# Kernel tuning notes

Hardware: AMD Instinct MI355X
Metric: run time of the kernel (lower is better)

## Reference

```python
import jax, jax.numpy as jnp
import numpy as np

N_NODES = 100000


def gcn_conv(x, src, dst, W, b, n_nodes):
    """PyG GCNConv: add self-loops, symmetric deg^{-1/2} norm, gather-scatter."""
    h = x @ W  # [N, out]
    # add self-loops (fixed shapes)
    loop = jnp.arange(n_nodes, dtype=src.dtype)
    s = jnp.concatenate([src, loop])
    d = jnp.concatenate([dst, loop])
    # degree on destination (includes self-loop)
    deg = jax.ops.segment_sum(jnp.ones_like(d, dtype=h.dtype), d, num_segments=n_nodes)
    dinv = jnp.where(deg > 0, jax.lax.rsqrt(deg), 0.0)
    norm = dinv[s] * dinv[d]  # [E+N]
    msg = h[s] * norm[:, None]  # gather + scale, [E+N, out]
    out = jax.ops.segment_sum(msg, d, num_segments=n_nodes)  # scatter-add
    return out + b


def setup_inputs() -> dict:
    key = jax.random.key(0)
    ks = jax.random.split(key, 10)
    n, in_d, hid, out_d, e = N_NODES, 64, 128, 64, 1600000
    x = jax.random.normal(ks[0], (n, in_d), dtype=jnp.float32)
    edge_index = jax.random.randint(ks[1], (2, e), 0, n, dtype=jnp.int64)
    s = 0.05
    return {
        "x": x,
        "edge_index": edge_index,
        "W1": jax.random.normal(ks[2], (in_d, hid), dtype=jnp.float32) * s,
        "b1": jnp.zeros((hid,), dtype=jnp.float32),
        "W2": jax.random.normal(ks[3], (hid, out_d), dtype=jnp.float32) * s,
        "b2": jnp.zeros((out_d,), dtype=jnp.float32),
        "Wd": jax.random.normal(ks[4], (out_d, 1), dtype=jnp.float32) * s,
        "bd": jnp.zeros((1,), dtype=jnp.float32),
        "Wp": jax.random.normal(ks[5], (out_d, 1), dtype=jnp.float32) * s,
        "bp": jnp.zeros((1,), dtype=jnp.float32),
    }


def reference(x, edge_index, W1, b1, W2, b2, Wd, bd, Wp, bp):
    src, dst = edge_index[0], edge_index[1]
    n = x.shape[0]
    h = jax.nn.relu(gcn_conv(x, src, dst, W1, b1, n))
    h = jax.nn.relu(gcn_conv(h, src, dst, W2, b2, n))
    duration_out = h @ Wd + bd  # [N, 1]
    phase_out = h @ Wp + bp     # [N, 1]
    return (duration_out, phase_out)
```

## Files before the change

kernel.cpp:

```cpp
#include <hip/hip_runtime.h>
#include <cstdint>
#include <cstddef>


#define MAXC 512
#define CAP  6144
#define SEG  3456
#define GPAD 16

typedef __attribute__((ext_vector_type(8))) short bf16x8;
typedef __attribute__((ext_vector_type(4))) float f32x4;

__device__ __forceinline__ float blo(unsigned int u) {
  return __uint_as_float(u << 16);
}
__device__ __forceinline__ float bhi(unsigned int u) {
  return __uint_as_float(u & 0xffff0000u);
}
__device__ __forceinline__ unsigned short f2b(float f) {
  unsigned int u = __float_as_uint(f);
  unsigned int r = u + 0x7fffu + ((u >> 16) & 1u);
  return (unsigned short)(r >> 16);
}

__device__ __forceinline__ void gacc(const uint2* __restrict__ tab,
                                     const int* __restrict__ cp,
                                     int m, int q, float4& acc) {
  int nfull = m & ~7;
  int t = 0;
  if (nfull) {
    int cb[8];
#pragma unroll
    for (int i = 0; i < 8; ++i) cb[i] = cp[i];
    for (t = 0; t < nfull; t += 8) {
      int ca[8];
#pragma unroll
      for (int i = 0; i < 8; ++i) ca[i] = cb[i];
      int tn = t + 8;
      if (tn < nfull) {
#pragma unroll
        for (int i = 0; i < 8; ++i) cb[i] = cp[tn + i];
      }
      uint2 v[8];
#pragma unroll
      for (int i = 0; i < 8; ++i) v[i] = tab[(size_t)ca[i] * 16 + q];
      acc.x += ((blo(v[0].x) + blo(v[1].x)) + (blo(v[2].x) + blo(v[3].x)))
             + ((blo(v[4].x) + blo(v[5].x)) + (blo(v[6].x) + blo(v[7].x)));
      acc.y += ((bhi(v[0].x) + bhi(v[1].x)) + (bhi(v[2].x) + bhi(v[3].x)))
             + ((bhi(v[4].x) + bhi(v[5].x)) + (bhi(v[6].x) + bhi(v[7].x)));
      acc.z += ((blo(v[0].y) + blo(v[1].y)) + (blo(v[2].y) + blo(v[3].y)))
             + ((blo(v[4].y) + blo(v[5].y)) + (blo(v[6].y) + blo(v[7].y)));
      acc.w += ((bhi(v[0].y) + bhi(v[1].y)) + (bhi(v[2].y) + bhi(v[3].y)))
             + ((bhi(v[4].y) + bhi(v[5].y)) + (bhi(v[6].y) + bhi(v[7].y)));
    }
  }
  if (t + 4 <= m) {
    int i0 = cp[t], i1 = cp[t + 1], i2 = cp[t + 2], i3 = cp[t + 3];
    uint2 v0 = tab[(size_t)i0 * 16 + q], v1 = tab[(size_t)i1 * 16 + q];
    uint2 v2 = tab[(size_t)i2 * 16 + q], v3 = tab[(size_t)i3 * 16 + q];
    acc.x += (blo(v0.x) + blo(v1.x)) + (blo(v2.x) + blo(v3.x));
    acc.y += (bhi(v0.x) + bhi(v1.x)) + (bhi(v2.x) + bhi(v3.x));
    acc.z += (blo(v0.y) + blo(v1.y)) + (blo(v2.y) + blo(v3.y));
    acc.w += (bhi(v0.y) + bhi(v1.y)) + (bhi(v2.y) + bhi(v3.y));
    t += 4;
  }
  for (; t < m; ++t) {
    int i0 = cp[t];
    uint2 v0 = tab[(size_t)i0 * 16 + q];
    acc.x += blo(v0.x); acc.y += bhi(v0.x);
    acc.z += blo(v0.y); acc.w += bhi(v0.y);
  }
}

__global__ void k_binit(int* __restrict__ gcur, int nc) {
  int b = blockIdx.x * 256 + threadIdx.x;
  if (b < nc) gcur[b * GPAD] = b * CAP;
}

__global__ __launch_bounds__(256) void k_pass1(const int* __restrict__ src,
                                               const int* __restrict__ dst,
                                               int* __restrict__ gcur,
                                               int* __restrict__ P,
                                               int E, int nc, int seg) {
  __shared__ int hist[MAXC];
  __shared__ int lofs[MAXC];
  __shared__ int base[MAXC];
  __shared__ int sbuf[SEG];
  __shared__ unsigned short dbuf[SEG];
  __shared__ int ssc[256];
  int tid = threadIdx.x;
  int start = blockIdx.x * seg;
  int end = min(E, start + seg);
  int cnt = end - start;
  if (cnt <= 0) return;
  for (int i = tid; i < MAXC; i += 256) hist[i] = 0;
  __syncthreads();
  for (int i = start + tid; i < end; i += 256)
    atomicAdd(&hist[dst[i] >> 8], 1);
  __syncthreads();
  int p0 = hist[2 * tid], p1 = hist[2 * tid + 1];
  int ps = p0 + p1;
  ssc[tid] = ps;
  __syncthreads();
  for (int off = 1; off < 256; off <<= 1) {
    int t = (tid >= off) ? ssc[tid - off] : 0;
    __syncthreads();
    ssc[tid] += t;
    __syncthreads();
  }
  int pe = ssc[tid] - ps;
  lofs[2 * tid] = pe;
  lofs[2 * tid + 1] = pe + p0;
  __syncthreads();
  for (int b = tid; b < nc; b += 256) {
    int h = hist[b];
    base[b] = (h ? atomicAdd(&gcur[b * GPAD], h) : 0) - lofs[b];
  }
  __syncthreads();
  for (int i = tid; i < MAXC; i += 256) hist[i] = lofs[i];
  __syncthreads();
  for (int i = start + tid; i < end; i += 256) {
    int d = dst[i];
    int b = d >> 8;
    int r = atomicAdd(&hist[b], 1);
    sbuf[r] = src[i] | ((d & 255) << 17);
    dbuf[r] = (unsigned short)b;
  }
  __syncthreads();
  for (int j = tid; j < cnt; j += 256) {
    P[base[dbuf[j]] + j] = sbuf[j];
  }
}

__global__ __launch_bounds__(256) void k_pass2(const int* __restrict__ P,
                                               const int* __restrict__ gcur,
                                               int* __restrict__ rs,
                                               int* __restrict__ c,
                                               float* __restrict__ dinv,
                                               int* __restrict__ col,
                                               const float* __restrict__ x,
                                               unsigned int* __restrict__ xh,
                                               int N) {
  __shared__ int sh[256];
  __shared__ int lcur[256];
  __shared__ float sdi[256];
  int tid = threadIdx.x;
  int node0 = blockIdx.x << 8;
  int begin = blockIdx.x * CAP;
  int end = gcur[blockIdx.x * GPAD];
  sh[tid] = 0;
  __syncthreads();
  for (int i = begin + tid; i < end; i += 256)
    atomicAdd(&sh[P[i] >> 17], 1);
  __syncthreads();
  int s = sh[tid];
  for (int off = 1; off < 256; off <<= 1) {
    int t = (tid >= off) ? sh[tid - off] : 0;
    __syncthreads();
    sh[tid] += t;
    __syncthreads();
  }
  int excl = sh[tid] - s;
  int node = node0 + tid;
  float di = rsqrtf((float)(s + 1));
  sdi[tid] = di;
  if (node < N) {
    rs[node] = begin + excl;
    c[node] = s;
    dinv[node] = di;
  }
  lcur[tid] = begin + excl;
  __syncthreads();
  for (int i = begin + tid; i < end; i += 256) {
    int p = P[i];
    int pos = atomicAdd(&lcur[p >> 17], 1);
    col[pos] = p & 0x1FFFF;
  }
  int nrem = min(256, N - node0);
  if (nrem <= 0) return;
  for (int i = tid; i < nrem * 16; i += 256) {
    int r = i >> 4, qq = i & 15;
    float d2 = sdi[r];
    float4 v = reinterpret_cast<const float4*>(x)[(size_t)(node0 + r) * 16 + qq];
    uint2 o;
    o.x = (unsigned int)f2b(v.x * d2) | ((unsigned int)f2b(v.y * d2) << 16);
    o.y = (unsigned int)f2b(v.z * d2) | ((unsigned int)f2b(v.w * d2) << 16);
    reinterpret_cast<uint2*>(xh)[(size_t)(node0 + r) * 16 + qq] = o;
  }
}

__global__ __launch_bounds__(256) void k_pull1(const unsigned int* __restrict__ xh,
                                               const int* __restrict__ rs,
                                               const int* __restrict__ cnt,
                                               const int* __restrict__ col,
                                               const float* __restrict__ dinv,
                                               unsigned int* __restrict__ aggh,
                                               int n) {
  int tid = threadIdx.x;
  int q = tid & 15;
  int node = (blockIdx.x * 256 + tid) >> 4;
  bool valid = node < n;
  int nidx = valid ? node : 0;
  int start = rs[nidx];
  int m = valid ? cnt[nidx] : 0;
  const uint2* xr = reinterpret_cast<const uint2*>(xh);
  float4 acc = {0.f, 0.f, 0.f, 0.f};
  gacc(xr, col + start, m, q, acc);
  if (valid) {
    uint2 sv = xr[(size_t)node * 16 + q];
    acc.x += blo(sv.x); acc.y += bhi(sv.x);
    acc.z += blo(sv.y); acc.w += bhi(sv.y);
    float di = dinv[node];
    uint2 o;
    o.x = (unsigned int)f2b(acc.x * di) | ((unsigned int)f2b(acc.y * di) << 16);
    o.y = (unsigned int)f2b(acc.z * di) | ((unsigned int)f2b(acc.w * di) << 16);
    reinterpret_cast<uint2*>(aggh)[(size_t)node * 16 + q] = o;
  }
}

#define OFF_W1T 16384
#define OFF_W2T 32768
#define OFF_H1  49152
__global__ __launch_bounds__(256) void k_gemm12(
    const unsigned int* __restrict__ aggh,
    const float* __restrict__ W1, const float* __restrict__ b1,
    const float* __restrict__ W2, const float* __restrict__ dinv,
    unsigned int* __restrict__ g2h, int n) {
  __shared__ __align__(16) char smem[81920];
  int tid = threadIdx.x;
  int lane = tid & 63;
  int wid = tid >> 6;
  int lr = lane & 15, lg = lane >> 4;
  int wr = wid >> 1, wc = wid & 1;
  {
    int nrow = tid >> 1, h = tid & 1;
    unsigned int pk[16];
#pragma unroll
    for (int q = 0; q < 16; ++q) {
      unsigned short a = f2b(W1[(size_t)(h * 32 + 2 * q) * 128 + nrow]);
      unsigned short bq = f2b(W1[(size_t)(h * 32 + 2 * q + 1) * 128 + nrow]);
      pk[q] = (unsigned int)a | ((unsigned int)bq << 16);
    }
#pragma unroll
    for (int cc = 0; cc < 4; ++cc) {
      uint4 v = make_uint4(pk[cc * 4], pk[cc * 4 + 1], pk[cc * 4 + 2], pk[cc * 4 + 3]);
      int byte = nrow * 128 + ((h * 64 + cc * 16) ^ ((nrow & 7) << 4));
      *reinterpret_cast<uint4*>(smem + OFF_W1T + byte) = v;
    }
  }
  {
    int nrow = tid >> 2, qt = tid & 3;
    unsigned int pk[16];
#pragma unroll
    for (int q = 0; q < 16; ++q) {
      unsigned short a = f2b(W2[(size_t)(qt * 32 + 2 * q) * 64 + nrow]);
      unsigned short bq = f2b(W2[(size_t)(qt * 32 + 2 * q + 1) * 64 + nrow]);
      pk[q] = (unsigned int)a | ((unsigned int)bq << 16);
    }
#pragma unroll
    for (int cc = 0; cc < 4; ++cc) {
      uint4 v = make_uint4(pk[cc * 4], pk[cc * 4 + 1], pk[cc * 4 + 2], pk[cc * 4 + 3]);
      int byte = nrow * 256 + ((qt * 64 + cc * 16) ^ ((nrow & 7) << 4));
      *reinterpret_cast<uint4*>(smem + OFF_W2T + byte) = v;
    }
  }
  float bias[4];
#pragma unroll
  for (int ni = 0; ni < 4; ++ni) bias[ni] = b1[wc * 64 + ni * 16 + lr];

  int ntiles = (n + 127) >> 7;
  for (int tile = blockIdx.x; tile < ntiles; tile += gridDim.x) {
    int row0 = tile << 7;
    __syncthreads();
#pragma unroll
    for (int j = 0; j < 4; ++j) {
      int idx = tid + 256 * j;
      int r = idx >> 3, u = idx & 7;
      uint4 v = make_uint4(0u, 0u, 0u, 0u);
      int row = row0 + r;
      if (row < n) v = reinterpret_cast<const uint4*>(aggh)[(size_t)row * 8 + u];
      int byte = r * 128 + ((u * 16) ^ ((r & 7) << 4));
      *reinterpret_cast<uint4*>(smem + byte) = v;
    }
    __syncthreads();
    f32x4 acc1[4][4];
#pragma unroll
    for (int mi = 0; mi < 4; ++mi)
#pragma unroll
      for (int ni = 0; ni < 4; ++ni) {
        f32x4 z = {0.f, 0.f, 0.f, 0.f};
        acc1[mi][ni] = z;
      }
#pragma unroll
    for (int kk = 0; kk < 2; ++kk) {
      int kb = kk * 64 + lg * 16;
      bf16x8 af[4], bfq[4];
#pragma unroll
      for (int mi = 0; mi < 4; ++mi) {
        int r = wr * 64 + mi * 16 + lr;
        af[mi] = *reinterpret_cast<const bf16x8*>(smem + r * 128 + (kb ^ ((r & 7) << 4)));
      }
#pragma unroll
      for (int ni = 0; ni < 4; ++ni) {
        int nr = wc * 64 + ni * 16 + lr;
        bfq[ni] = *reinterpret_cast<const bf16x8*>(smem + OFF_W1T + nr * 128 + (kb ^ ((nr & 7) << 4)));
      }
#pragma unroll
      for (int mi = 0; mi < 4; ++mi)
#pragma unroll
        for (int ni = 0; ni < 4; ++ni)
          acc1[mi][ni] = __builtin_amdgcn_mfma_f32_16x16x32_bf16(
              af[mi], bfq[ni], acc1[mi][ni], 0, 0, 0);
    }
#pragma unroll
    for (int mi = 0; mi < 4; ++mi) {
      int m0 = wr * 64 + mi * 16 + lg * 4;
#pragma unroll
      for (int ni = 0; ni < 4; ++ni) {
        int kcol = wc * 64 + ni * 16 + lr;
#pragma unroll
        for (int rj = 0; rj < 4; ++rj) {
          float v = fmaxf(acc1[mi][ni][rj] + bias[ni], 0.f);
          int mm = m0 + rj;
          int byte = mm * 256 + ((kcol * 2) ^ ((mm & 15) << 4));
          *reinterpret_cast<unsigned short*>(smem + OFF_H1 + byte) = f2b(v);
        }
      }
    }
    __syncthreads();
    f32x4 acc2[4][2];
#pragma unroll
    for (int mi = 0; mi < 4; ++mi)
#pragma unroll
      for (int ni = 0; ni < 2; ++ni) {
        f32x4 z = {0.f, 0.f, 0.f, 0.f};
        acc2[mi][ni] = z;
      }
#pragma unroll
    for (int kk = 0; kk < 4; ++kk) {
      int kb = kk * 64 + lg * 16;
      bf16x8 af[4], bfq[2];
#pragma unroll
      for (int mi = 0; mi < 4; ++mi) {
        int m = wr * 64 + mi * 16 + lr;
        af[mi] = *reinterpret_cast<const bf16x8*>(smem + OFF_H1 + m * 256 + (kb ^ ((m & 15) << 4)));
      }
#pragma unroll
      for (int ni = 0; ni < 2; ++ni) {
        int nr = wc * 32 + ni * 16 + lr;
        bfq[ni] = *reinterpret_cast<const bf16x8*>(smem + OFF_W2T + nr * 256 + (kb ^ ((nr & 7) << 4)));
      }
#pragma unroll
      for (int mi = 0; mi < 4; ++mi)
#pragma unroll
        for (int ni = 0; ni < 2; ++ni)
          acc2[mi][ni] = __builtin_amdgcn_mfma_f32_16x16x32_bf16(
              af[mi], bfq[ni], acc2[mi][ni], 0, 0, 0);
    }
    __syncthreads();
#pragma unroll
    for (int mi = 0; mi < 4; ++mi) {
      int m0 = wr * 64 + mi * 16 + lg * 4;
#pragma unroll
      for (int ni = 0; ni < 2; ++ni) {
        int nn = wc * 32 + ni * 16 + lr;
#pragma unroll
        for (int rj = 0; rj < 4; ++rj) {
          int mm = m0 + rj;
          int byte = mm * 256 + ((nn * 4) ^ ((mm & 15) << 4));
          *reinterpret_cast<float*>(smem + OFF_H1 + byte) = acc2[mi][ni][rj];
        }
      }
    }
    __syncthreads();
#pragma unroll
    for (int j = 0; j < 8; ++j) {
      int idx = tid + 256 * j;
      int r = idx >> 4, c4 = idx & 15;
      int row = row0 + r;
      if (row < n) {
        float4 v = *reinterpret_cast<const float4*>(
            smem + OFF_H1 + r * 256 + ((c4 * 16) ^ ((r & 15) << 4)));
        float di = dinv[row];
        uint2 o;
        o.x = (unsigned int)f2b(v.x * di) | ((unsigned int)f2b(v.y * di) << 16);
        o.y = (unsigned int)f2b(v.z * di) | ((unsigned int)f2b(v.w * di) << 16);
        reinterpret_cast<uint2*>(g2h)[(size_t)row * 16 + c4] = o;
      }
    }
  }
}

__global__ __launch_bounds__(256) void k_pull2(const unsigned int* __restrict__ g2h,
                                               const int* __restrict__ rs,
                                               const int* __restrict__ cnt,
                                               const int* __restrict__ col,
                                               const float* __restrict__ dinv,
                                               const float* __restrict__ b,
                                               const float* __restrict__ Wd,
                                               const float* __restrict__ Wp,
                                               const float* __restrict__ bd,
                                               const float* __restrict__ bp,
                                               float* __restrict__ out, int n) {
  int tid = threadIdx.x;
  int q = tid & 15;
  int node = (blockIdx.x * 256 + tid) >> 4;
  bool valid = node < n;
  int nidx = valid ? node : 0;
  int start = rs[nidx];
  int m = valid ? cnt[nidx] : 0;
  const uint2* gr = reinterpret_cast<const uint2*>(g2h);
  float4 acc = {0.f, 0.f, 0.f, 0.f};
  gacc(gr, col + start, m, q, acc);
  {
    uint2 sv = gr[(size_t)nidx * 16 + q];
    acc.x += blo(sv.x); acc.y += bhi(sv.x);
    acc.z += blo(sv.y); acc.w += bhi(sv.y);
  }
  float di = dinv[nidx];
  float4 b4 = *reinterpret_cast<const float4*>(b + q * 4);
  float4 wd4 = *reinterpret_cast<const float4*>(Wd + q * 4);
  float4 wp4 = *reinterpret_cast<const float4*>(Wp + q * 4);
  float vx = fmaxf(fmaf(acc.x, di, b4.x), 0.f);
  float vy = fmaxf(fmaf(acc.y, di, b4.y), 0.f);
  float vz = fmaxf(fmaf(acc.z, di, b4.z), 0.f);
  float vw = fmaxf(fmaf(acc.w, di, b4.w), 0.f);
  float dsum = vx * wd4.x + vy * wd4.y + vz * wd4.z + vw * wd4.w;
  float psum = vx * wp4.x + vy * wp4.y + vz * wp4.z + vw * wp4.w;
#pragma unroll
  for (int off = 1; off < 16; off <<= 1) {
    dsum += __shfl_xor(dsum, off);
    psum += __shfl_xor(psum, off);
  }
  if (valid && q == 0) {
    out[node] = dsum + bd[0];
    out[n + node] = psum + bp[0];
  }
}

extern "C" void kernel_launch(void* const* d_in, const int* in_sizes, int n_in,
                              void* d_out, int out_size, void* d_ws, size_t ws_size,
                              hipStream_t stream) {
  const float* x  = (const float*)d_in[0];
  const int*   ei = (const int*)d_in[1];
  const float* W1 = (const float*)d_in[2];
  const float* b1 = (const float*)d_in[3];
  const float* W2 = (const float*)d_in[4];
  const float* b2 = (const float*)d_in[5];
  const float* Wd = (const float*)d_in[6];
  const float* bd = (const float*)d_in[7];
  const float* Wp = (const float*)d_in[8];
  const float* bp = (const float*)d_in[9];
  float* out = (float*)d_out;

  const int N = in_sizes[0] / 64;
  const int E = in_sizes[1] / 2;
  const int* src = ei;
  const int* dst = ei + E;
  const int nc = (N + 255) >> 8;

  char* ws = (char*)d_ws;
  size_t off = 0;
  auto alloc = [&](size_t bytes) -> void* {
    size_t a = (off + 255) & ~(size_t)255;
    off = a + bytes;
    return (void*)(ws + a);
  };

  int*   gcur = (int*)alloc((size_t)MAXC * GPAD * 4);
  int*   rs   = (int*)alloc((size_t)N * 4);
  int*   c    = (int*)alloc((size_t)N * 4);
  float* dinv = (float*)alloc((size_t)N * 4);
  int*   P    = (int*)alloc((size_t)nc * CAP * 4);
  int*   col  = (int*)alloc((size_t)nc * CAP * 4);
  unsigned int* xh   = (unsigned int*)alloc((size_t)N * 64 * 2);
  unsigned int* aggh = (unsigned int*)alloc((size_t)N * 64 * 2);
  unsigned int* g2h  = (unsigned int*)alloc((size_t)N * 64 * 2);
  (void)ws_size; (void)n_in; (void)out_size;

  k_binit<<<(nc + 255) / 256, 256, 0, stream>>>(gcur, nc);

  int nb1 = 512;
  int seg = (E + nb1 - 1) / nb1;
  while (seg > SEG) { nb1 *= 2; seg = (E + nb1 - 1) / nb1; }
  k_pass1<<<nb1, 256, 0, stream>>>(src, dst, gcur, P, E, nc, seg);
  k_pass2<<<nc, 256, 0, stream>>>(P, gcur, rs, c, dinv, col, x, xh, N);

  k_pull1<<<(N + 15) / 16, 256, 0, stream>>>(xh, rs, c, col, dinv, aggh, N);
  k_gemm12<<<512, 256, 0, stream>>>(aggh, W1, b1, W2, dinv, g2h, N);
  k_pull2<<<(N + 15) / 16, 256, 0, stream>>>(g2h, rs, c, col, dinv, b2, Wd, Wp, bd, bp, out, N);
}
```

Before: 223.2 us.

## Widen gather loads to 16 bytes, use wave-shuffle scans, replace init kernel with memset

```diff
diff --git a/kernel.cpp b/kernel.cpp
--- a/kernel.cpp
+++ b/kernel.cpp
@@ -23,58 +23,52 @@
   return (unsigned short)(r >> 16);
 }
 
-__device__ __forceinline__ void gacc(const uint2* __restrict__ tab,
-                                     const int* __restrict__ cp,
-                                     int m, int q, float4& acc) {
-  int nfull = m & ~7;
+__device__ __forceinline__ void gacc8(const uint4* __restrict__ tab,
+                                      const int* __restrict__ cp,
+                                      int m, int q8, float a[8]) {
   int t = 0;
-  if (nfull) {
-    int cb[8];
-#pragma unroll
-    for (int i = 0; i < 8; ++i) cb[i] = cp[i];
-    for (t = 0; t < nfull; t += 8) {
-      int ca[8];
-#pragma unroll
-      for (int i = 0; i < 8; ++i) ca[i] = cb[i];
-      int tn = t + 8;
-      if (tn < nfull) {
-#pragma unroll
-        for (int i = 0; i < 8; ++i) cb[i] = cp[tn + i];
-      }
-      uint2 v[8];
-#pragma unroll
-      for (int i = 0; i < 8; ++i) v[i] = tab[(size_t)ca[i] * 16 + q];
-      acc.x += ((blo(v[0].x) + blo(v[1].x)) + (blo(v[2].x) + blo(v[3].x)))
-             + ((blo(v[4].x) + blo(v[5].x)) + (blo(v[6].x) + blo(v[7].x)));
-      acc.y += ((bhi(v[0].x) + bhi(v[1].x)) + (bhi(v[2].x) + bhi(v[3].x)))
-             + ((bhi(v[4].x) + bhi(v[5].x)) + (bhi(v[6].x) + bhi(v[7].x)));
-      acc.z += ((blo(v[0].y) + blo(v[1].y)) + (blo(v[2].y) + blo(v[3].y)))
-             + ((blo(v[4].y) + blo(v[5].y)) + (blo(v[6].y) + blo(v[7].y)));
-      acc.w += ((bhi(v[0].y) + bhi(v[1].y)) + (bhi(v[2].y) + bhi(v[3].y)))
-             + ((bhi(v[4].y) + bhi(v[5].y)) + (bhi(v[6].y) + bhi(v[7].y)));
-    }
-  }
-  if (t + 4 <= m) {
-    int i0 = cp[t], i1 = cp[t + 1], i2 = cp[t + 2], i3 = cp[t + 3];
-    uint2 v0 = tab[(size_t)i0 * 16 + q], v1 = tab[(size_t)i1 * 16 + q];
-    uint2 v2 = tab[(size_t)i2 * 16 + q], v3 = tab[(size_t)i3 * 16 + q];
-    acc.x += (blo(v0.x) + blo(v1.x)) + (blo(v2.x) + blo(v3.x));
-    acc.y += (bhi(v0.x) + bhi(v1.x)) + (bhi(v2.x) + bhi(v3.x));
-    acc.z += (blo(v0.y) + blo(v1.y)) + (blo(v2.y) + blo(v3.y));
-    acc.w += (bhi(v0.y) + bhi(v1.y)) + (bhi(v2.y) + bhi(v3.y));
-    t += 4;
+  for (; t + 8 <= m; t += 8) {
+    int c0 = cp[t],     c1 = cp[t + 1], c2 = cp[t + 2], c3 = cp[t + 3];
+    int c4 = cp[t + 4], c5 = cp[t + 5], c6 = cp[t + 6], c7 = cp[t + 7];
+    uint4 v0 = tab[(size_t)c0 * 8 + q8], v1 = tab[(size_t)c1 * 8 + q8];
+    uint4 v2 = tab[(size_t)c2 * 8 + q8], v3 = tab[(size_t)c3 * 8 + q8];
+    uint4 v4 = tab[(size_t)c4 * 8 + q8], v5 = tab[(size_t)c5 * 8 + q8];
+    uint4 v6 = tab[(size_t)c6 * 8 + q8], v7 = tab[(size_t)c7 * 8 + q8];
+    a[0] += ((blo(v0.x) + blo(v1.x)) + (blo(v2.x) + blo(v3.x)))
+          + ((blo(v4.x) + blo(v5.x)) + (blo(v6.x) + blo(v7.x)));
+    a[1] += ((bhi(v0.x) + bhi(v1.x)) + (bhi(v2.x) + bhi(v3.x)))
+          + ((bhi(v4.x) + bhi(v5.x)) + (bhi(v6.x) + bhi(v7.x)));
+    a[2] += ((blo(v0.y) + blo(v1.y)) + (blo(v2.y) + blo(v3.y)))
+          + ((blo(v4.y) + blo(v5.y)) + (blo(v6.y) + blo(v7.y)));
+    a[3] += ((bhi(v0.y) + bhi(v1.y)) + (bhi(v2.y) + bhi(v3.y)))
+          + ((bhi(v4.y) + bhi(v5.y)) + (bhi(v6.y) + bhi(v7.y)));
+    a[4] += ((blo(v0.z) + blo(v1.z)) + (blo(v2.z) + blo(v3.z)))
+          + ((blo(v4.z) + blo(v5.z)) + (blo(v6.z) + blo(v7.z)));
+    a[5] += ((bhi(v0.z) + bhi(v1.z)) + (bhi(v2.z) + bhi(v3.z)))
+          + ((bhi(v4.z) + bhi(v5.z)) + (bhi(v6.z) + bhi(v7.z)));
+    a[6] += ((blo(v0.w) + blo(v1.w)) + (blo(v2.w) + blo(v3.w)))
+          + ((blo(v4.w) + blo(v5.w)) + (blo(v6.w) + blo(v7.w)));
+    a[7] += ((bhi(v0.w) + bhi(v1.w)) + (bhi(v2.w) + bhi(v3.w)))
+          + ((bhi(v4.w) + bhi(v5.w)) + (bhi(v6.w) + bhi(v7.w)));
+  }
+  for (; t + 4 <= m; t += 4) {
+    int c0 = cp[t], c1 = cp[t + 1], c2 = cp[t + 2], c3 = cp[t + 3];
+    uint4 v0 = tab[(size_t)c0 * 8 + q8], v1 = tab[(size_t)c1 * 8 + q8];
+    uint4 v2 = tab[(size_t)c2 * 8 + q8], v3 = tab[(size_t)c3 * 8 + q8];
+    a[0] += (blo(v0.x) + blo(v1.x)) + (blo(v2.x) + blo(v3.x));
+    a[1] += (bhi(v0.x) + bhi(v1.x)) + (bhi(v2.x) + bhi(v3.x));
+    a[2] += (blo(v0.y) + blo(v1.y)) + (blo(v2.y) + blo(v3.y));
+    a[3] += (bhi(v0.y) + bhi(v1.y)) + (bhi(v2.y) + bhi(v3.y));
+    a[4] += (blo(v0.z) + blo(v1.z)) + (blo(v2.z) + blo(v3.z));
+    a[5] += (bhi(v0.z) + bhi(v1.z)) + (bhi(v2.z) + bhi(v3.z));
+    a[6] += (blo(v0.w) + blo(v1.w)) + (blo(v2.w) + blo(v3.w));
+    a[7] += (bhi(v0.w) + bhi(v1.w)) + (bhi(v2.w) + bhi(v3.w));
   }
   for (; t < m; ++t) {
-    int i0 = cp[t];
-    uint2 v0 = tab[(size_t)i0 * 16 + q];
-    acc.x += blo(v0.x); acc.y += bhi(v0.x);
-    acc.z += blo(v0.y); acc.w += bhi(v0.y);
-  }
-}
-
-__global__ void k_binit(int* __restrict__ gcur, int nc) {
-  int b = blockIdx.x * 256 + threadIdx.x;
-  if (b < nc) gcur[b * GPAD] = b * CAP;
+    uint4 v = tab[(size_t)cp[t] * 8 + q8];
+    a[0] += blo(v.x); a[1] += bhi(v.x); a[2] += blo(v.y); a[3] += bhi(v.y);
+    a[4] += blo(v.z); a[5] += bhi(v.z); a[6] += blo(v.w); a[7] += bhi(v.w);
+  }
 }
 
 __global__ __launch_bounds__(256) void k_pass1(const int* __restrict__ src,
@@ -87,8 +81,9 @@
   __shared__ int base[MAXC];
   __shared__ int sbuf[SEG];
   __shared__ unsigned short dbuf[SEG];
-  __shared__ int ssc[256];
+  __shared__ int wsum[4];
   int tid = threadIdx.x;
+  int lane = tid & 63, wv = tid >> 6;
   int start = blockIdx.x * seg;
   int end = min(E, start + seg);
   int cnt = end - start;
@@ -100,21 +95,26 @@
   __syncthreads();
   int p0 = hist[2 * tid], p1 = hist[2 * tid + 1];
   int ps = p0 + p1;
-  ssc[tid] = ps;
-  __syncthreads();
-  for (int off = 1; off < 256; off <<= 1) {
-    int t = (tid >= off) ? ssc[tid - off] : 0;
-    __syncthreads();
-    ssc[tid] += t;
-    __syncthreads();
-  }
-  int pe = ssc[tid] - ps;
+  int incl = ps;
+#pragma unroll
+  for (int off = 1; off < 64; off <<= 1) {
+    int t = __shfl_up(incl, off);
+    if (lane >= off) incl += t;
+  }
+  if (lane == 63) wsum[wv] = incl;
+  __syncthreads();
+  int addv = 0;
+#pragma unroll
+  for (int w = 0; w < 3; ++w)
+    if (w < wv) addv += wsum[w];
+  incl += addv;
+  int pe = incl - ps;
   lofs[2 * tid] = pe;
   lofs[2 * tid + 1] = pe + p0;
   __syncthreads();
   for (int b = tid; b < nc; b += 256) {
     int h = hist[b];
-    base[b] = (h ? atomicAdd(&gcur[b * GPAD], h) : 0) - lofs[b];
+    base[b] = (h ? (b * CAP + atomicAdd(&gcur[b * GPAD], h)) : 0) - lofs[b];
   }
   __syncthreads();
   for (int i = tid; i < MAXC; i += 256) hist[i] = lofs[i];
@@ -144,23 +144,32 @@
   __shared__ int sh[256];
   __shared__ int lcur[256];
   __shared__ float sdi[256];
+  __shared__ int wsum[4];
   int tid = threadIdx.x;
+  int lane = tid & 63, wv = tid >> 6;
   int node0 = blockIdx.x << 8;
   int begin = blockIdx.x * CAP;
-  int end = gcur[blockIdx.x * GPAD];
+  int end = begin + gcur[blockIdx.x * GPAD];
   sh[tid] = 0;
   __syncthreads();
   for (int i = begin + tid; i < end; i += 256)
     atomicAdd(&sh[P[i] >> 17], 1);
   __syncthreads();
   int s = sh[tid];
-  for (int off = 1; off < 256; off <<= 1) {
-    int t = (tid >= off) ? sh[tid - off] : 0;
-    __syncthreads();
-    sh[tid] += t;
-    __syncthreads();
-  }
-  int excl = sh[tid] - s;
+  int incl = s;
+#pragma unroll
+  for (int off = 1; off < 64; off <<= 1) {
+    int t = __shfl_up(incl, off);
+    if (lane >= off) incl += t;
+  }
+  if (lane == 63) wsum[wv] = incl;
+  __syncthreads();
+  int addv = 0;
+#pragma unroll
+  for (int w = 0; w < 3; ++w)
+    if (w < wv) addv += wsum[w];
+  incl += addv;
+  int excl = incl - s;
   int node = node0 + tid;
   float di = rsqrtf((float)(s + 1));
   sdi[tid] = di;
@@ -197,24 +206,26 @@
                                                unsigned int* __restrict__ aggh,
                                                int n) {
   int tid = threadIdx.x;
-  int q = tid & 15;
-  int node = (blockIdx.x * 256 + tid) >> 4;
+  int q8 = tid & 7;
+  int node = (blockIdx.x * 256 + tid) >> 3;
   bool valid = node < n;
   int nidx = valid ? node : 0;
   int start = rs[nidx];
   int m = valid ? cnt[nidx] : 0;
-  const uint2* xr = reinterpret_cast<const uint2*>(xh);
-  float4 acc = {0.f, 0.f, 0.f, 0.f};
-  gacc(xr, col + start, m, q, acc);
+  const uint4* xr = reinterpret_cast<const uint4*>(xh);
+  float a[8] = {0.f, 0.f, 0.f, 0.f, 0.f, 0.f, 0.f, 0.f};
+  gacc8(xr, col + start, m, q8, a);
   if (valid) {
-    uint2 sv = xr[(size_t)node * 16 + q];
-    acc.x += blo(sv.x); acc.y += bhi(sv.x);
-    acc.z += blo(sv.y); acc.w += bhi(sv.y);
+    uint4 sv = xr[(size_t)node * 8 + q8];
+    a[0] += blo(sv.x); a[1] += bhi(sv.x); a[2] += blo(sv.y); a[3] += bhi(sv.y);
+    a[4] += blo(sv.z); a[5] += bhi(sv.z); a[6] += blo(sv.w); a[7] += bhi(sv.w);
     float di = dinv[node];
-    uint2 o;
-    o.x = (unsigned int)f2b(acc.x * di) | ((unsigned int)f2b(acc.y * di) << 16);
-    o.y = (unsigned int)f2b(acc.z * di) | ((unsigned int)f2b(acc.w * di) << 16);
-    reinterpret_cast<uint2*>(aggh)[(size_t)node * 16 + q] = o;
+    uint4 o;
+    o.x = (unsigned int)f2b(a[0] * di) | ((unsigned int)f2b(a[1] * di) << 16);
+    o.y = (unsigned int)f2b(a[2] * di) | ((unsigned int)f2b(a[3] * di) << 16);
+    o.z = (unsigned int)f2b(a[4] * di) | ((unsigned int)f2b(a[5] * di) << 16);
+    o.w = (unsigned int)f2b(a[6] * di) | ((unsigned int)f2b(a[7] * di) << 16);
+    reinterpret_cast<uint4*>(aggh)[(size_t)node * 8 + q8] = o;
   }
 }
 
@@ -403,36 +414,45 @@
                                                const float* __restrict__ bp,
                                                float* __restrict__ out, int n) {
   int tid = threadIdx.x;
-  int q = tid & 15;
-  int node = (blockIdx.x * 256 + tid) >> 4;
+  int q8 = tid & 7;
+  int node = (blockIdx.x * 256 + tid) >> 3;
   bool valid = node < n;
   int nidx = valid ? node : 0;
   int start = rs[nidx];
   int m = valid ? cnt[nidx] : 0;
-  const uint2* gr = reinterpret_cast<const uint2*>(g2h);
-  float4 acc = {0.f, 0.f, 0.f, 0.f};
-  gacc(gr, col + start, m, q, acc);
+  const uint4* gr = reinterpret_cast<const uint4*>(g2h);
+  float a[8] = {0.f, 0.f, 0.f, 0.f, 0.f, 0.f, 0.f, 0.f};
+  gacc8(gr, col + start, m, q8, a);
   {
-    uint2 sv = gr[(size_t)nidx * 16 + q];
-    acc.x += blo(sv.x); acc.y += bhi(sv.x);
-    acc.z += blo(sv.y); acc.w += bhi(sv.y);
+    uint4 sv = gr[(size_t)nidx * 8 + q8];
+    a[0] += blo(sv.x); a[1] += bhi(sv.x); a[2] += blo(sv.y); a[3] += bhi(sv.y);
+    a[4] += blo(sv.z); a[5] += bhi(sv.z); a[6] += blo(sv.w); a[7] += bhi(sv.w);
   }
   float di = dinv[nidx];
-  float4 b4 = *reinterpret_cast<const float4*>(b + q * 4);
-  float4 wd4 = *reinterpret_cast<const float4*>(Wd + q * 4);
-  float4 wp4 = *reinterpret_cast<const float4*>(Wp + q * 4);
-  float vx = fmaxf(fmaf(acc.x, di, b4.x), 0.f);
-  float vy = fmaxf(fmaf(acc.y, di, b4.y), 0.f);
-  float vz = fmaxf(fmaf(acc.z, di, b4.z), 0.f);
-  float vw = fmaxf(fmaf(acc.w, di, b4.w), 0.f);
-  float dsum = vx * wd4.x + vy * wd4.y + vz * wd4.z + vw * wd4.w;
-  float psum = vx * wp4.x + vy * wp4.y + vz * wp4.z + vw * wp4.w;
-#pragma unroll
-  for (int off = 1; off < 16; off <<= 1) {
+  float4 bA = *reinterpret_cast<const float4*>(b + q8 * 8);
+  float4 bB = *reinterpret_cast<const float4*>(b + q8 * 8 + 4);
+  float4 wdA = *reinterpret_cast<const float4*>(Wd + q8 * 8);
+  float4 wdB = *reinterpret_cast<const float4*>(Wd + q8 * 8 + 4);
+  float4 wpA = *reinterpret_cast<const float4*>(Wp + q8 * 8);
+  float4 wpB = *reinterpret_cast<const float4*>(Wp + q8 * 8 + 4);
+  float v0 = fmaxf(fmaf(a[0], di, bA.x), 0.f);
+  float v1 = fmaxf(fmaf(a[1], di, bA.y), 0.f);
+  float v2 = fmaxf(fmaf(a[2], di, bA.z), 0.f);
+  float v3 = fmaxf(fmaf(a[3], di, bA.w), 0.f);
+  float v4 = fmaxf(fmaf(a[4], di, bB.x), 0.f);
+  float v5 = fmaxf(fmaf(a[5], di, bB.y), 0.f);
+  float v6 = fmaxf(fmaf(a[6], di, bB.z), 0.f);
+  float v7 = fmaxf(fmaf(a[7], di, bB.w), 0.f);
+  float dsum = ((v0 * wdA.x + v1 * wdA.y) + (v2 * wdA.z + v3 * wdA.w))
+             + ((v4 * wdB.x + v5 * wdB.y) + (v6 * wdB.z + v7 * wdB.w));
+  float psum = ((v0 * wpA.x + v1 * wpA.y) + (v2 * wpA.z + v3 * wpA.w))
+             + ((v4 * wpB.x + v5 * wpB.y) + (v6 * wpB.z + v7 * wpB.w));
+#pragma unroll
+  for (int off = 1; off < 8; off <<= 1) {
     dsum += __shfl_xor(dsum, off);
     psum += __shfl_xor(psum, off);
   }
-  if (valid && q == 0) {
+  if (valid && q8 == 0) {
     out[node] = dsum + bd[0];
     out[n + node] = psum + bp[0];
   }
@@ -478,7 +498,7 @@
   unsigned int* g2h  = (unsigned int*)alloc((size_t)N * 64 * 2);
   (void)ws_size; (void)n_in; (void)out_size;
 
-  k_binit<<<(nc + 255) / 256, 256, 0, stream>>>(gcur, nc);
+  hipMemsetAsync(gcur, 0, (size_t)MAXC * GPAD * 4, stream);
 
   int nb1 = 512;
   int seg = (E + nb1 - 1) / nb1;
@@ -486,7 +506,7 @@
   k_pass1<<<nb1, 256, 0, stream>>>(src, dst, gcur, P, E, nc, seg);
   k_pass2<<<nc, 256, 0, stream>>>(P, gcur, rs, c, dinv, col, x, xh, N);
 
-  k_pull1<<<(N + 15) / 16, 256, 0, stream>>>(xh, rs, c, col, dinv, aggh, N);
+  k_pull1<<<(N + 31) / 32, 256, 0, stream>>>(xh, rs, c, col, dinv, aggh, N);
   k_gemm12<<<512, 256, 0, stream>>>(aggh, W1, b1, W2, dinv, g2h, N);
-  k_pull2<<<(N + 15) / 16, 256, 0, stream>>>(g2h, rs, c, col, dinv, b2, Wd, Wp, bd, bp, out, N);
-}
+  k_pull2<<<(N + 31) / 32, 256, 0, stream>>>(g2h, rs, c, col, dinv, b2, Wd, Wp, bd, bp, out, N);
+}
```

Measured after the change: 220.3 us. No clear change (-1.3%).
